# Optimization experiments

Hardware: AMD Instinct MI355X
Metric: run time of the kernel (lower is better)

The kernel has to match this reference:

```python
import jax, jax.numpy as jnp
import numpy as np

B, S, D, H = 8, 1024, 768, 12
C = D // H  # head dim = 64
NEG_SLOPE = 0.2  # PyG GATConv default leaky_relu slope


def setup_inputs() -> dict:
    key = jax.random.key(0)
    ks = jax.random.split(key, 12)
    s = 0.02
    return {
        "hidden_states": jax.random.normal(ks[0], (B, S, D), jnp.float32),
        "transformer_output": jax.random.normal(ks[1], (B, S, D), jnp.float32),
        # GATConv params: lin (no bias), att_src/att_dst [H, C], bias [H*C]
        "W_gat": jax.random.normal(ks[2], (D, D), jnp.float32) * s,
        "att_src": jax.random.normal(ks[3], (H, C), jnp.float32) * s,
        "att_dst": jax.random.normal(ks[4], (H, C), jnp.float32) * s,
        "b_gat": jnp.zeros((D,), jnp.float32),
        # gat_projection
        "W_proj": jax.random.normal(ks[5], (D, D), jnp.float32) * s,
        "b_proj": jnp.zeros((D,), jnp.float32),
        # fusion
        "W_fus": jax.random.normal(ks[6], (2 * D, D), jnp.float32) * s,
        "b_fus": jnp.zeros((D,), jnp.float32),
    }


def reference(hidden_states, transformer_output, W_gat, att_src, att_dst,
              b_gat, W_proj, b_proj, W_fus, b_fus):
    # --- GATConv on a fully-connected graph (+ default self-loops) ---
    # Fully connected + self loops => softmax over ALL sources per target,
    # so the scatter-softmax reduces to dense attention.
    x = (hidden_states @ W_gat).reshape(B, S, H, C)          # [B,S,H,C]
    a_src = jnp.einsum('bshc,hc->bhs', x, att_src)           # score contribution of source j
    a_dst = jnp.einsum('bshc,hc->bhs', x, att_dst)           # score contribution of target i
    # scores[b,h,i,j] = a_dst_i + a_src_j, then leaky_relu, softmax over j
    scores = jax.nn.leaky_relu(a_dst[:, :, :, None] + a_src[:, :, None, :],
                               negative_slope=NEG_SLOPE)     # [B,H,S,S]
    attn = jax.nn.softmax(scores, axis=-1)
    out = jnp.einsum('bhij,bjhc->bihc', attn, x)             # aggregate sources
    gat_out = out.reshape(B, S, D) + b_gat                   # concat heads + bias

    # --- projection, fusion ---
    graph_output = gat_out @ W_proj + b_proj
    fused = jnp.concatenate([transformer_output, graph_output], axis=-1)
    fused = fused @ W_fus + b_fus
    return fused
```

## Files before the change

### kernel.cpp

```cpp
#include <hip/hip_runtime.h>
#include <hip/hip_bf16.h>

#define NB 8
#define NS 1024
#define ND 768
#define NH 12
#define NC 64
#define NEG 0.2f
#define NBUK 128

typedef __attribute__((ext_vector_type(8))) short bf16x8;
typedef __attribute__((ext_vector_type(4))) float f32x4;

static __device__ __forceinline__ float bf2f(unsigned short u) {
    union { float f; unsigned int i; } v; v.i = ((unsigned int)u) << 16; return v.f;
}
static __device__ __forceinline__ unsigned short f2bf(float f) {
    union { float f; unsigned int i; } v; v.f = f;
    unsigned int r = v.i + 0x7FFFu + ((v.i >> 16) & 1u);
    return (unsigned short)(r >> 16);
}

static __device__ __forceinline__ void gload16(const unsigned short* g, unsigned short* l) {
    __builtin_amdgcn_global_load_lds((const __attribute__((address_space(1))) void*)g,
                                     (__attribute__((address_space(3))) void*)l, 16, 0, 0);
}

static __device__ __forceinline__ int swz_bid(int orig, int nwg) {
    int q = nwg >> 3, r = nwg & 7;
    int xcd = orig & 7, idx = orig >> 3;
    return (xcd < r ? xcd * (q + 1) : r * (q + 1) + (xcd - r) * q) + idx;
}

__global__ __launch_bounds__(256) void k_prep(const float* __restrict__ hs, const float* __restrict__ to,
                                              const float* __restrict__ Wp, const float* __restrict__ Wg,
                                              const float* __restrict__ Wf, const float* __restrict__ bp,
                                              const float* __restrict__ bfu,
                                              unsigned short* __restrict__ h_bf, unsigned short* __restrict__ t_bf,
                                              unsigned short* __restrict__ Wp_bf, unsigned short* __restrict__ WgT,
                                              unsigned short* __restrict__ WfT, float* __restrict__ bias_tot,
                                              int n1, int n2) {
    const int NT1 = (ND / 32) * (3 * ND / 32);
    const int NT2 = (ND * 8) / 256;
    int blk = blockIdx.x, t = threadIdx.x;
    if (blk < NT1) {
        __shared__ float tile[32][33];
        int bx = blk % (ND / 32), by = blk / (ND / 32);
        const float* src; unsigned short* dst; int K, k0;
        if (by < ND / 32) { src = Wg; dst = WgT; K = ND; k0 = by * 32; }
        else { src = Wf; dst = WfT; K = 2 * ND; k0 = (by - ND / 32) * 32; }
        int n0 = bx * 32;
        int r = t >> 3, c4 = (t & 7) * 4;
        float4 v = *reinterpret_cast<const float4*>(src + (size_t)(k0 + r) * ND + n0 + c4);
        tile[r][c4] = v.x; tile[r][c4 + 1] = v.y; tile[r][c4 + 2] = v.z; tile[r][c4 + 3] = v.w;
        __syncthreads();
        ushort4 o;
        o.x = f2bf(tile[c4][r]); o.y = f2bf(tile[c4 + 1][r]);
        o.z = f2bf(tile[c4 + 2][r]); o.w = f2bf(tile[c4 + 3][r]);
        *reinterpret_cast<ushort4*>(dst + (size_t)(n0 + r) * K + k0 + c4) = o;
    } else if (blk < NT1 + NT2) {
        int gid = (blk - NT1) * 256 + t;
        int c = gid >> 3, sl = gid & 7;
        float acc = 0.f;
        int k0 = sl * 96;
#pragma unroll 8
        for (int k = k0; k < k0 + 96; k++) acc += bp[k] * Wf[(size_t)(ND + k) * ND + c];
        acc += __shfl_down(acc, 1, 64);
        acc += __shfl_down(acc, 2, 64);
        acc += __shfl_down(acc, 4, 64);
        if (sl == 0) bias_tot[c] = acc + bfu[c];
    } else {
        int gid = (blk - NT1 - NT2) * 256 + t;
        const float* s; unsigned short* d; int i;
        if (gid < n1) { s = hs; d = h_bf; i = gid; }
        else if (gid < 2 * n1) { s = to; d = t_bf; i = gid - n1; }
        else { s = Wp; d = Wp_bf; i = gid - 2 * n1; if (i >= n2) return; }
        i *= 4;
        float4 v = *reinterpret_cast<const float4*>(s + i);
        ushort4 o;
        o.x = f2bf(v.x); o.y = f2bf(v.y); o.z = f2bf(v.z); o.w = f2bf(v.w);
        *reinterpret_cast<ushort4*>(d + i) = o;
    }
}

__global__ __launch_bounds__(256) void k_bucket(const float* __restrict__ a_src,
                                                float4* __restrict__ pack,
                                                int* __restrict__ bstart,
                                                float* __restrict__ smax_g,
                                                float2* __restrict__ bparam,
                                                float* __restrict__ zb) {
    int bh = blockIdx.x, t = threadIdx.x;
    __shared__ float v[1024];
    __shared__ int bi[1024];
    __shared__ float red[256];
    __shared__ int cnt[NBUK], pre[NBUK];
    __shared__ float zs1[NBUK], zs2[NBUK];
    for (int i = t; i < 1024; i += 256) v[i] = a_src[(size_t)bh * 1024 + i];
    if (t < NBUK) { cnt[t] = 0; zs1[t] = 0.f; zs2[t] = 0.f; }
    __syncthreads();
    float lm = -1e30f, ln = 1e30f;
    for (int i = t; i < 1024; i += 256) { lm = fmaxf(lm, v[i]); ln = fminf(ln, v[i]); }
    red[t] = lm; __syncthreads();
    for (int s = 128; s > 0; s >>= 1) { if (t < s) red[t] = fmaxf(red[t], red[t + s]); __syncthreads(); }
    float mx = red[0]; __syncthreads();
    red[t] = ln; __syncthreads();
    for (int s = 128; s > 0; s >>= 1) { if (t < s) red[t] = fminf(red[t], red[t + s]); __syncthreads(); }
    float mn = red[0]; __syncthreads();
    float scale = (float)NBUK / fmaxf(mx - mn, 1e-20f);
    for (int i = t; i < 1024; i += 256) {
        int bk = (int)((v[i] - mn) * scale);
        bk = min(max(bk, 0), NBUK - 1);
        bi[i] = bk;
        atomicAdd(&cnt[bk], 1);
    }
    __syncthreads();
    if (t < NBUK) pre[t] = cnt[t];
    __syncthreads();
    for (int off = 1; off < NBUK; off <<= 1) {
        int x = (t >= off && t < NBUK) ? pre[t - off] : 0;
        __syncthreads();
        if (t < NBUK) pre[t] += x;
        __syncthreads();
    }
    if (t < NBUK) {
        int start = pre[t] - cnt[t];
        bstart[bh * (NBUK + 1) + t] = start;
        cnt[t] = start;
    }
    if (t == 0) {
        bstart[bh * (NBUK + 1) + NBUK] = 1024;
        smax_g[bh] = mx;
        bparam[bh] = make_float2(mn, scale);
    }
    __syncthreads();
    for (int i = t; i < 1024; i += 256) {
        int pos = atomicAdd(&cnt[bi[i]], 1);
        float u = v[i] - mx;
        float4 p;
        p.x = u; p.y = __expf(u); p.z = __expf(0.2f * u); p.w = __int_as_float(i);
        pack[(size_t)bh * 1024 + pos] = p;
        atomicAdd(&zs1[bi[i]], p.y);
        atomicAdd(&zs2[bi[i]], p.z);
    }
    __syncthreads();
    for (int off = 1; off < NBUK; off <<= 1) {
        float x1 = (t >= off && t < NBUK) ? zs1[t - off] : 0.f;
        float x2 = (t >= off && t < NBUK) ? zs2[t - off] : 0.f;
        __syncthreads();
        if (t < NBUK) { zs1[t] += x1; zs2[t] += x2; }
        __syncthreads();
    }
    if (t < NBUK) {
        zb[(size_t)(bh * NBUK + t) * 2] = zs1[t];
        zb[(size_t)(bh * NBUK + t) * 2 + 1] = zs2[t];
    }
}

__global__ __launch_bounds__(256) void k_bsum(const unsigned short* __restrict__ x_bf,
                                              const float4* __restrict__ pack,
                                              const int* __restrict__ bstart,
                                              float* __restrict__ P) {
    int grp = blockIdx.x, bh = blockIdx.y;
    int t = threadIdx.x, w = t >> 6, lane = t & 63;
    int b = bh / NH, h = bh % NH;
    const float4* pk = pack + (size_t)bh * 1024;
    const unsigned short* xb = x_bf + (size_t)b * NS * ND + h * 64 + lane;
#pragma unroll
    for (int r = 0; r < 2; r++) {
        int bk = grp * 8 + w * 2 + r;
        int ks = bstart[bh * (NBUK + 1) + bk], ke = bstart[bh * (NBUK + 1) + bk + 1];
        float V1 = 0.f, V2 = 0.f;
        for (int k = ks; k < ke; k++) {
            float4 p = pk[k];
            int j = __float_as_int(p.w);
            float xv = bf2f(xb[(size_t)j * ND]);
            V1 += p.y * xv; V2 += p.z * xv;
        }
        size_t o = ((size_t)(bh * NBUK + bk) * 2) * 64 + lane;
        P[o] = V1; P[o + 64] = V2;
    }
}

__global__ __launch_bounds__(256) void k_bpref(float* __restrict__ P) {
    int bh = blockIdx.x, t = threadIdx.x, w = t >> 6, lane = t & 63;
    __shared__ float segV[4][2][64];
    size_t base = (size_t)bh * NBUK;
    float V1 = 0.f, V2 = 0.f;
    for (int g = 0; g < 4; ++g) {
        float a1[8], a2[8];
#pragma unroll
        for (int r = 0; r < 8; r++) {
            size_t o = ((base + w * 32 + g * 8 + r) * 2) * 64 + lane;
            a1[r] = P[o]; a2[r] = P[o + 64];
        }
#pragma unroll
        for (int r = 0; r < 8; r++) { V1 += a1[r]; a1[r] = V1; V2 += a2[r]; a2[r] = V2; }
#pragma unroll
        for (int r = 0; r < 8; r++) {
            size_t o = ((base + w * 32 + g * 8 + r) * 2) * 64 + lane;
            P[o] = a1[r]; P[o + 64] = a2[r];
        }
    }
    segV[w][0][lane] = V1; segV[w][1][lane] = V2;
    __syncthreads();
    if (w > 0) {
        float O1 = 0.f, O2 = 0.f;
        for (int w2 = 0; w2 < w; w2++) { O1 += segV[w2][0][lane]; O2 += segV[w2][1][lane]; }
        for (int g = 0; g < 4; ++g) {
            float a1[8], a2[8];
#pragma unroll
            for (int r = 0; r < 8; r++) {
                size_t o = ((base + w * 32 + g * 8 + r) * 2) * 64 + lane;
                a1[r] = P[o]; a2[r] = P[o + 64];
            }
#pragma unroll
            for (int r = 0; r < 8; r++) {
                size_t o = ((base + w * 32 + g * 8 + r) * 2) * 64 + lane;
                P[o] = a1[r] + O1; P[o + 64] = a2[r] + O2;
            }
        }
    }
}

__global__ __launch_bounds__(256) void k_apply3(const float* __restrict__ P,
                                                const float* __restrict__ zb,
                                                const float* __restrict__ a_dst,
                                                const float* __restrict__ smax_g,
                                                const float2* __restrict__ bparam,
                                                const float* __restrict__ b_gat,
                                                unsigned short* __restrict__ gat) {
    int bh = blockIdx.y, t = threadIdx.x, w = t >> 6, lane = t & 63;
    int b = bh / NH, h = bh % NH;
    float sm = smax_g[bh];
    float2 bp_ = bparam[bh];
    float mn = bp_.x, scale = bp_.y;
    size_t pb = (size_t)bh * NBUK;
    float T1 = P[((pb + NBUK - 1) * 2) * 64 + lane];
    float z1tot = zb[(pb + NBUK - 1) * 2];
    float bias = b_gat[h * 64 + lane];
#pragma unroll
    for (int q = 0; q < 8; q++) {
        int i = blockIdx.x * 32 + w * 8 + q;
        float d = a_dst[(size_t)bh * 1024 + i];
        float dm = d + sm;
        float m = dm > 0.f ? dm : NEG * dm;
        float c1 = __expf(dm - m);
        float c2 = __expf(NEG * dm - m);
        int e = (int)floorf((-d - mn) * scale + 0.5f);
        e = min(max(e, 0), NBUK);
        float P1f = 0.f, P2f = 0.f, z1f = 0.f, z2f = 0.f;
        if (e > 0) {
            size_t o = ((pb + e - 1) * 2) * 64 + lane;
            P1f = P[o]; P2f = P[o + 64];
            z1f = zb[(pb + e - 1) * 2];
            z2f = zb[(pb + e - 1) * 2 + 1];
        }
        float num = c1 * (T1 - P1f) + c2 * P2f;
        float Z = c1 * (z1tot - z1f) + c2 * z2f;
        gat[((size_t)(b * NS + i)) * ND + h * 64 + lane] = f2bf(num / Z + bias);
    }
}

template <bool OUT_BF16, bool BIAS, bool DUAL, bool ATT>
static __device__ __forceinline__ void gemm_body(
    const unsigned short* __restrict__ A1, const unsigned short* __restrict__ B1,
    int lda1, int ldb1,
    const unsigned short* __restrict__ A2, const unsigned short* __restrict__ B2,
    int lda2, int ldb2,
    const float* __restrict__ bias, void* __restrict__ Cout,
    int m0, int n0, int N, int K,
    unsigned short* sA, unsigned short* sB,
    const float* __restrict__ att_src, const float* __restrict__ att_dst,
    float* __restrict__ a_src, float* __restrict__ a_dst) {
    int t = threadIdx.x, wave = t >> 6, lane = t & 63;
    int lr = lane & 15, kq = lane >> 4;
    int srow = t >> 3;
    int scol = ((t & 7) ^ (srow & 7)) * 8;
    int cs0 = ((kq) ^ (lr & 7)) * 8;
    int cs1 = ((4 + kq) ^ (lr & 7)) * 8;
    const int kh = K >> 6;
    const int nsteps = (DUAL ? 2 : 1) * kh;
    f32x4 acc[4][2] = {};

    auto STAGE = [&](int s, int buf) {
        const unsigned short* A; const unsigned short* Bt; int lda, ldb, k0;
        if (DUAL && s >= kh) { A = A2; Bt = B2; lda = lda2; ldb = ldb2; k0 = (s - kh) << 6; }
        else { A = A1; Bt = B1; lda = lda1; ldb = ldb1; k0 = s << 6; }
        const unsigned short* gA = A + (size_t)(m0 + srow) * lda + scol + k0;
        const unsigned short* gB = Bt + (size_t)(n0 + srow) * ldb + scol + k0;
        unsigned short* dA = sA + buf * 4096 + t * 8;
        unsigned short* dB = sB + buf * 8192 + t * 8;
        gload16(gA, dA);
        gload16(gA + (size_t)32 * lda, dA + 2048);
        gload16(gB, dB);
        gload16(gB + (size_t)32 * ldb, dB + 2048);
        gload16(gB + (size_t)64 * ldb, dB + 4096);
        gload16(gB + (size_t)96 * ldb, dB + 6144);
    };
    auto COMPUTE = [&](int cur) {
        unsigned short* cA = sA + cur * 4096;
        unsigned short* cB = sB + cur * 8192;
        bf16x8 a0[4], a1v[4], b0[2], b1v[2];
#pragma unroll
        for (int m = 0; m < 4; m++) {
            a0[m]  = *reinterpret_cast<bf16x8*>(&cA[(m * 16 + lr) * 64 + cs0]);
            a1v[m] = *reinterpret_cast<bf16x8*>(&cA[(m * 16 + lr) * 64 + cs1]);
        }
#pragma unroll
        for (int n = 0; n < 2; n++) {
            b0[n]  = *reinterpret_cast<bf16x8*>(&cB[(wave * 32 + n * 16 + lr) * 64 + cs0]);
            b1v[n] = *reinterpret_cast<bf16x8*>(&cB[(wave * 32 + n * 16 + lr) * 64 + cs1]);
        }
#pragma unroll
        for (int m = 0; m < 4; m++)
#pragma unroll
            for (int n = 0; n < 2; n++) {
                acc[m][n] = __builtin_amdgcn_mfma_f32_16x16x32_bf16(a0[m], b0[n], acc[m][n], 0, 0, 0);
                acc[m][n] = __builtin_amdgcn_mfma_f32_16x16x32_bf16(a1v[m], b1v[n], acc[m][n], 0, 0, 0);
            }
    };

    STAGE(0, 0);
    STAGE(1, 1);
    for (int s = 0; s < nsteps - 1; s++) {
        int cur = s & 1;
        asm volatile("s_waitcnt vmcnt(6)" ::: "memory");
        __builtin_amdgcn_s_barrier();
        __builtin_amdgcn_sched_barrier(0);
        COMPUTE(cur);
        __builtin_amdgcn_sched_barrier(0);
        __builtin_amdgcn_s_barrier();
        if (s + 2 < nsteps) STAGE(s + 2, cur);
    }
    asm volatile("s_waitcnt vmcnt(0)" ::: "memory");
    __builtin_amdgcn_s_barrier();
    __builtin_amdgcn_sched_barrier(0);
    COMPUTE((nsteps - 1) & 1);

    int rg = kq * 4;
#pragma unroll
    for (int m = 0; m < 4; m++) {
#pragma unroll
        for (int n = 0; n < 2; n++) {
            int col = n0 + wave * 32 + n * 16 + lr;
            float bv = BIAS ? bias[col] : 0.0f;
#pragma unroll
            for (int r = 0; r < 4; r++) {
                int row = m0 + m * 16 + rg + r;
                float v = acc[m][n][r] + bv;
                if (OUT_BF16) {
                    ((unsigned short*)Cout)[(size_t)row * N + col] = f2bf(v);
                } else {
                    ((float*)Cout)[(size_t)row * N + col] = v;
                }
            }
        }
    }

    if (ATT) {
        __syncthreads();
        float ds_[4][4] = {}, dd_[4][4] = {};
#pragma unroll
        for (int n = 0; n < 2; n++) {
            int colg = n0 + wave * 32 + n * 16 + lr;
            float as_v = att_src[colg];
            float ad_v = att_dst[colg];
#pragma unroll
            for (int m = 0; m < 4; m++)
#pragma unroll
                for (int r = 0; r < 4; r++) {
                    ds_[m][r] = fmaf(acc[m][n][r], as_v, ds_[m][r]);
                    dd_[m][r] = fmaf(acc[m][n][r], ad_v, dd_[m][r]);
                }
        }
#pragma unroll
        for (int off = 1; off <= 8; off <<= 1)
#pragma unroll
            for (int m = 0; m < 4; m++)
#pragma unroll
                for (int r = 0; r < 4; r++) {
                    ds_[m][r] += __shfl_xor(ds_[m][r], off, 64);
                    dd_[m][r] += __shfl_xor(dd_[m][r], off, 64);
                }
        float* red = (float*)sA;
        if (lr == 0) {
#pragma unroll
            for (int m = 0; m < 4; m++)
#pragma unroll
                for (int r = 0; r < 4; r++) {
                    int rl = m * 16 + kq * 4 + r;
                    red[wave * 64 + rl] = ds_[m][r];
                    red[256 + wave * 64 + rl] = dd_[m][r];
                }
        }
        __syncthreads();
        if (t < 128) {
            int hb = t >> 6, rl = t & 63;
            float vs = red[(hb * 2) * 64 + rl] + red[(hb * 2 + 1) * 64 + rl];
            float vd = red[256 + (hb * 2) * 64 + rl] + red[256 + (hb * 2 + 1) * 64 + rl];
            int grow = m0 + rl;
            int b = grow >> 10, sdx = grow & 1023;
            int head = (n0 >> 6) + hb;
            a_src[((size_t)b * NH + head) * NS + sdx] = vs;
            a_dst[((size_t)b * NH + head) * NS + sdx] = vd;
        }
    }
}

__global__ __launch_bounds__(256) void k_gemm_pair(
    const unsigned short* __restrict__ Aa, const unsigned short* __restrict__ Ba,
    unsigned short* __restrict__ Ca, int NBna, int Na, int Ka, int lda_a, int ldb_a, int nwg_a,
    const unsigned short* __restrict__ Ab, const unsigned short* __restrict__ Bb,
    unsigned short* __restrict__ Cb, int NBnb, int Nb, int Kb, int lda_b, int ldb_b,
    const float* __restrict__ att_src, const float* __restrict__ att_dst,
    float* __restrict__ a_src, float* __restrict__ a_dst) {
    __shared__ alignas(16) unsigned short sA[2 * 64 * 64];
    __shared__ alignas(16) unsigned short sB[2 * 128 * 64];
    int wg = swz_bid(blockIdx.x, gridDim.x);
    if (wg < nwg_a) {
        gemm_body<true, false, false, true>(Aa, Ba, lda_a, ldb_a, nullptr, nullptr, 0, 0, nullptr,
                                            Ca, (wg / NBna) * 64, (wg % NBna) * 128, Na, Ka, sA, sB,
                                            att_src, att_dst, a_src, a_dst);
    } else {
        wg -= nwg_a;
        gemm_body<true, false, false, false>(Ab, Bb, lda_b, ldb_b, nullptr, nullptr, 0, 0, nullptr,
                                             Cb, (wg / NBnb) * 64, (wg % NBnb) * 128, Nb, Kb, sA, sB,
                                             nullptr, nullptr, nullptr, nullptr);
    }
}

__global__ __launch_bounds__(256) void k_gemm_dual(
    const unsigned short* __restrict__ A1, const unsigned short* __restrict__ B1,
    const unsigned short* __restrict__ A2, const unsigned short* __restrict__ B2,
    const float* __restrict__ bias, float* __restrict__ out,
    int NBn, int N, int K, int lda, int ldb1, int ldb2) {
    __shared__ alignas(16) unsigned short sA[2 * 64 * 64];
    __shared__ alignas(16) unsigned short sB[2 * 128 * 64];
    int wg = swz_bid(blockIdx.x, gridDim.x);
    gemm_body<false, true, true, false>(A1, B1, lda, ldb1, A2, B2, lda, ldb2, bias,
                                        out, (wg / NBn) * 64, (wg % NBn) * 128, N, K, sA, sB,
                                        nullptr, nullptr, nullptr, nullptr);
}

extern "C" void kernel_launch(void* const* d_in, const int* in_sizes, int n_in,
                              void* d_out, int out_size, void* d_ws, size_t ws_size,
                              hipStream_t stream) {
    const float* hs  = (const float*)d_in[0];
    const float* to  = (const float*)d_in[1];
    const float* Wg  = (const float*)d_in[2];
    const float* asv = (const float*)d_in[3];
    const float* adv = (const float*)d_in[4];
    const float* bg  = (const float*)d_in[5];
    const float* Wp  = (const float*)d_in[6];
    const float* bp  = (const float*)d_in[7];
    const float* Wf  = (const float*)d_in[8];
    const float* bfu = (const float*)d_in[9];
    float* out = (float*)d_out;

    char* ws = (char*)d_ws;
    size_t off = 0;
    auto alloc = [&](size_t bytes) -> void* {
        void* p = ws + off;
        off = (off + bytes + 255) & ~(size_t)255;
        return p;
    };
    const size_t NBSD = (size_t)NB * NS * ND;
    const int NBH = NB * NH;
    unsigned short* h_bf   = (unsigned short*)alloc(NBSD * 2);
    unsigned short* x_bf   = (unsigned short*)alloc(NBSD * 2);
    unsigned short* t_bf   = (unsigned short*)alloc(NBSD * 2);
    unsigned short* WgT    = (unsigned short*)alloc((size_t)ND * ND * 2);
    unsigned short* Wp_bf  = (unsigned short*)alloc((size_t)ND * ND * 2);
    unsigned short* WfT    = (unsigned short*)alloc((size_t)2 * ND * ND * 2);
    unsigned short* WcombT = (unsigned short*)alloc((size_t)ND * ND * 2);
    float*  bias_tot = (float*)alloc((size_t)ND * 4);
    float*  a_src = (float*)alloc((size_t)NBH * NS * 4);
    float*  a_dst = (float*)alloc((size_t)NBH * NS * 4);
    float4* pack  = (float4*)alloc((size_t)NBH * NS * 16);
    int*    bstart = (int*)alloc((size_t)NBH * (NBUK + 1) * 4);
    float*  P     = (float*)alloc((size_t)NBH * NBUK * 2 * 64 * 4);
    float*  zb    = (float*)alloc((size_t)NBH * NBUK * 2 * 4);
    float*  smaxb = (float*)alloc((size_t)NBH * 4);
    float2* bparam = (float2*)alloc((size_t)NBH * 8);

    int n1 = (int)NBSD / 4, n2 = ND * ND / 4;
    const int NT1 = (ND / 32) * (3 * ND / 32);
    const int NT2 = (ND * 8) / 256;
    const int NT3 = (2 * n1 + n2 + 255) / 256;
    k_prep<<<NT1 + NT2 + NT3, 256, 0, stream>>>(hs, to, Wp, Wg, Wf, bp, bfu,
                                                h_bf, t_bf, Wp_bf, WgT, WfT, bias_tot, n1, n2);

    int nwg1 = (NB * NS / 64) * (ND / 128);
    int nwgW = (ND / 64) * (ND / 128);
    k_gemm_pair<<<nwg1 + nwgW, 256, 0, stream>>>(
        h_bf, WgT, x_bf, ND / 128, ND, ND, ND, ND, nwg1,
        WfT + ND, Wp_bf, WcombT, ND / 128, ND, ND, 2 * ND, ND,
        asv, adv, a_src, a_dst);

    k_bucket<<<NBH, 256, 0, stream>>>(a_src, pack, bstart, smaxb, bparam, zb);
    k_bsum<<<dim3(NBUK / 8, NBH), 256, 0, stream>>>(x_bf, pack, bstart, P);
    k_bpref<<<NBH, 256, 0, stream>>>(P);

    unsigned short* gat_bf = h_bf;
    k_apply3<<<dim3(NS / 32, NBH), 256, 0, stream>>>(P, zb, a_dst, smaxb, bparam, bg, gat_bf);

    k_gemm_dual<<<(NB * NS / 64) * (ND / 128), 256, 0, stream>>>(
        t_bf, WfT, gat_bf, WcombT, bias_tot, out, ND / 128, ND, ND, ND, 2 * ND, ND);
}
```

Before: 136.2 us.

## Fuse bucketing into bucket-sum kernel and triple-buffer GEMM pipeline

Merges k_bucket and k_bsum into one kernel. Each of the 16 blocks per (batch, head) recomputes the bucket sort in shared memory, so the packed float4 array and bucket starts no longer go through global memory and one launch is removed. The cost is redundant sorting work, repeated 16 times per head. Separately, the GEMM body moves from double to triple buffering of the A/B LDS tiles with a deeper vmcnt wait, which hides more load latency but raises LDS use per block and may reduce occupancy.

```diff
diff --git a/kernel.cpp b/kernel.cpp
--- a/kernel.cpp
+++ b/kernel.cpp
@@ -83,17 +83,19 @@
     }
 }
 
-__global__ __launch_bounds__(256) void k_bucket(const float* __restrict__ a_src,
-                                                float4* __restrict__ pack,
-                                                int* __restrict__ bstart,
-                                                float* __restrict__ smax_g,
-                                                float2* __restrict__ bparam,
-                                                float* __restrict__ zb) {
-    int bh = blockIdx.x, t = threadIdx.x;
+__global__ __launch_bounds__(256) void k_bsumf(const unsigned short* __restrict__ x_bf,
+                                               const float* __restrict__ a_src,
+                                               float* __restrict__ P,
+                                               float* __restrict__ zb,
+                                               float* __restrict__ smax_g,
+                                               float2* __restrict__ bparam) {
+    int grp = blockIdx.x, bh = blockIdx.y, t = threadIdx.x;
+    int b = bh / NH, h = bh % NH;
     __shared__ float v[1024];
-    __shared__ int bi[1024];
+    __shared__ float pe1[1024], pe2[1024];
+    __shared__ unsigned short pj[1024];
     __shared__ float red[256];
-    __shared__ int cnt[NBUK], pre[NBUK];
+    __shared__ int cnt[NBUK], pre[NBUK], ofs[NBUK], bst[NBUK + 1];
     __shared__ float zs1[NBUK], zs2[NBUK];
     for (int i = t; i < 1024; i += 256) v[i] = a_src[(size_t)bh * 1024 + i];
     if (t < NBUK) { cnt[t] = 0; zs1[t] = 0.f; zs2[t] = 0.f; }
@@ -108,9 +110,7 @@
     float mn = red[0]; __syncthreads();
     float scale = (float)NBUK / fmaxf(mx - mn, 1e-20f);
     for (int i = t; i < 1024; i += 256) {
-        int bk = (int)((v[i] - mn) * scale);
-        bk = min(max(bk, 0), NBUK - 1);
-        bi[i] = bk;
+        int bk = min(max((int)((v[i] - mn) * scale), 0), NBUK - 1);
         atomicAdd(&cnt[bk], 1);
     }
     __syncthreads();
@@ -124,23 +124,19 @@
     }
     if (t < NBUK) {
         int start = pre[t] - cnt[t];
-        bstart[bh * (NBUK + 1) + t] = start;
-        cnt[t] = start;
-    }
-    if (t == 0) {
-        bstart[bh * (NBUK + 1) + NBUK] = 1024;
-        smax_g[bh] = mx;
-        bparam[bh] = make_float2(mn, scale);
-    }
+        bst[t] = start;
+        ofs[t] = start;
+    }
+    if (t == 0) bst[NBUK] = 1024;
     __syncthreads();
     for (int i = t; i < 1024; i += 256) {
-        int pos = atomicAdd(&cnt[bi[i]], 1);
+        int bk = min(max((int)((v[i] - mn) * scale), 0), NBUK - 1);
         float u = v[i] - mx;
-        float4 p;
-        p.x = u; p.y = __expf(u); p.z = __expf(0.2f * u); p.w = __int_as_float(i);
-        pack[(size_t)bh * 1024 + pos] = p;
-        atomicAdd(&zs1[bi[i]], p.y);
-        atomicAdd(&zs2[bi[i]], p.z);
+        float e1 = __expf(u), e2 = __expf(0.2f * u);
+        int pos = atomicAdd(&ofs[bk], 1);
+        pe1[pos] = e1; pe2[pos] = e2; pj[pos] = (unsigned short)i;
+        atomicAdd(&zs1[bk], e1);
+        atomicAdd(&zs2[bk], e2);
     }
     __syncthreads();
     for (int off = 1; off < NBUK; off <<= 1) {
@@ -150,31 +146,24 @@
         if (t < NBUK) { zs1[t] += x1; zs2[t] += x2; }
         __syncthreads();
     }
-    if (t < NBUK) {
-        zb[(size_t)(bh * NBUK + t) * 2] = zs1[t];
-        zb[(size_t)(bh * NBUK + t) * 2 + 1] = zs2[t];
-    }
-}
-
-__global__ __launch_bounds__(256) void k_bsum(const unsigned short* __restrict__ x_bf,
-                                              const float4* __restrict__ pack,
-                                              const int* __restrict__ bstart,
-                                              float* __restrict__ P) {
-    int grp = blockIdx.x, bh = blockIdx.y;
-    int t = threadIdx.x, w = t >> 6, lane = t & 63;
-    int b = bh / NH, h = bh % NH;
-    const float4* pk = pack + (size_t)bh * 1024;
+    if (grp == 0) {
+        if (t < NBUK) {
+            zb[(size_t)(bh * NBUK + t) * 2] = zs1[t];
+            zb[(size_t)(bh * NBUK + t) * 2 + 1] = zs2[t];
+        }
+        if (t == 0) { smax_g[bh] = mx; bparam[bh] = make_float2(mn, scale); }
+    }
+    int w = t >> 6, lane = t & 63;
     const unsigned short* xb = x_bf + (size_t)b * NS * ND + h * 64 + lane;
 #pragma unroll
     for (int r = 0; r < 2; r++) {
         int bk = grp * 8 + w * 2 + r;
-        int ks = bstart[bh * (NBUK + 1) + bk], ke = bstart[bh * (NBUK + 1) + bk + 1];
+        int ks = bst[bk], ke = bst[bk + 1];
         float V1 = 0.f, V2 = 0.f;
         for (int k = ks; k < ke; k++) {
-            float4 p = pk[k];
-            int j = __float_as_int(p.w);
-            float xv = bf2f(xb[(size_t)j * ND]);
-            V1 += p.y * xv; V2 += p.z * xv;
+            float xv = bf2f(xb[(size_t)pj[k] * ND]);
+            V1 += pe1[k] * xv;
+            V2 += pe2[k] * xv;
         }
         size_t o = ((size_t)(bh * NBUK + bk) * 2) * 64 + lane;
         P[o] = V1; P[o + 64] = V2;
@@ -322,20 +311,25 @@
 
     STAGE(0, 0);
     STAGE(1, 1);
-    for (int s = 0; s < nsteps - 1; s++) {
-        int cur = s & 1;
-        asm volatile("s_waitcnt vmcnt(6)" ::: "memory");
+    STAGE(2, 2);
+    for (int s = 0; s < nsteps - 2; s++) {
+        int cur = s % 3;
+        asm volatile("s_waitcnt vmcnt(12)" ::: "memory");
         __builtin_amdgcn_s_barrier();
         __builtin_amdgcn_sched_barrier(0);
         COMPUTE(cur);
         __builtin_amdgcn_sched_barrier(0);
         __builtin_amdgcn_s_barrier();
-        if (s + 2 < nsteps) STAGE(s + 2, cur);
-    }
+        if (s + 3 < nsteps) STAGE(s + 3, cur);
+    }
+    asm volatile("s_waitcnt vmcnt(6)" ::: "memory");
+    __builtin_amdgcn_s_barrier();
+    __builtin_amdgcn_sched_barrier(0);
+    COMPUTE((nsteps - 2) % 3);
     asm volatile("s_waitcnt vmcnt(0)" ::: "memory");
     __builtin_amdgcn_s_barrier();
     __builtin_amdgcn_sched_barrier(0);
-    COMPUTE((nsteps - 1) & 1);
+    COMPUTE((nsteps - 1) % 3);
 
     int rg = kq * 4;
 #pragma unroll
@@ -414,8 +408,8 @@
     unsigned short* __restrict__ Cb, int NBnb, int Nb, int Kb, int lda_b, int ldb_b,
     const float* __restrict__ att_src, const float* __restrict__ att_dst,
     float* __restrict__ a_src, float* __restrict__ a_dst) {
-    __shared__ alignas(16) unsigned short sA[2 * 64 * 64];
-    __shared__ alignas(16) unsigned short sB[2 * 128 * 64];
+    __shared__ alignas(16) unsigned short sA[3 * 64 * 64];
+    __shared__ alignas(16) unsigned short sB[3 * 128 * 64];
     int wg = swz_bid(blockIdx.x, gridDim.x);
     if (wg < nwg_a) {
         gemm_body<true, false, false, true>(Aa, Ba, lda_a, ldb_a, nullptr, nullptr, 0, 0, nullptr,
@@ -434,8 +428,8 @@
     const unsigned short* __restrict__ A2, const unsigned short* __restrict__ B2,
     const float* __restrict__ bias, float* __restrict__ out,
     int NBn, int N, int K, int lda, int ldb1, int ldb2) {
-    __shared__ alignas(16) unsigned short sA[2 * 64 * 64];
-    __shared__ alignas(16) unsigned short sB[2 * 128 * 64];
+    __shared__ alignas(16) unsigned short sA[3 * 64 * 64];
+    __shared__ alignas(16) unsigned short sB[3 * 128 * 64];
     int wg = swz_bid(blockIdx.x, gridDim.x);
     gemm_body<false, true, true, false>(A1, B1, lda, ldb1, A2, B2, lda, ldb2, bias,
                                         out, (wg / NBn) * 64, (wg % NBn) * 128, N, K, sA, sB,
@@ -476,8 +470,6 @@
     float*  bias_tot = (float*)alloc((size_t)ND * 4);
     float*  a_src = (float*)alloc((size_t)NBH * NS * 4);
     float*  a_dst = (float*)alloc((size_t)NBH * NS * 4);
-    float4* pack  = (float4*)alloc((size_t)NBH * NS * 16);
-    int*    bstart = (int*)alloc((size_t)NBH * (NBUK + 1) * 4);
     float*  P     = (float*)alloc((size_t)NBH * NBUK * 2 * 64 * 4);
     float*  zb    = (float*)alloc((size_t)NBH * NBUK * 2 * 4);
     float*  smaxb = (float*)alloc((size_t)NBH * 4);
@@ -497,8 +489,7 @@
         WfT + ND, Wp_bf, WcombT, ND / 128, ND, ND, 2 * ND, ND,
         asv, adv, a_src, a_dst);
 
-    k_bucket<<<NBH, 256, 0, stream>>>(a_src, pack, bstart, smaxb, bparam, zb);
-    k_bsum<<<dim3(NBUK / 8, NBH), 256, 0, stream>>>(x_bf, pack, bstart, P);
+    k_bsumf<<<dim3(NBUK / 8, NBH), 256, 0, stream>>>(x_bf, a_src, P, zb, smaxb, bparam);
     k_bpref<<<NBH, 256, 0, stream>>>(P);
 
     unsigned short* gat_bf = h_bf;
```

New measurement: 150.3 us. 10.4% more time.
